# Kernel optimization log

Hardware: AMD Instinct MI355X
Metric: run time of the kernel (lower is better)

The kernel has to match this reference:

```python
import jax, jax.numpy as jnp
import numpy as np

B = 524288          # batch
C = 128             # num_classes
CONF_PEN = 0.5      # confusion_penalty coefficient
PROB_THRESH = 0.2   # wrong-prob threshold from original loop
WEIGHT_THRESH = 1.0 # weight threshold from original loop


def setup_inputs() -> dict:
    key = jax.random.key(0)
    k1, k2, k3 = jax.random.split(key, 3)
    # scale logits so softmax is peaky enough that the >0.2 branch fires
    outputs = 5.0 * jax.random.normal(k1, (B, C), dtype=jnp.float32)
    labels = jax.random.randint(k2, (B,), 0, C, dtype=jnp.int32)
    # uniform in [0, 2): roughly half the weights exceed the 1.0 threshold
    confusion_weights = jax.random.uniform(k3, (C, C), dtype=jnp.float32, minval=0.0, maxval=2.0)
    return {"outputs": outputs, "labels": labels, "confusion_weights": confusion_weights}


def reference(outputs, labels, confusion_weights):
    # base cross-entropy (mean over batch), numerically stable
    logp = jax.nn.log_softmax(outputs, axis=-1)                       # [B, C]
    base_loss = -jnp.take_along_axis(logp, labels[:, None].astype(jnp.int32), axis=1).mean()

    # confusion penalty (computed under no_grad in the original)
    probs = jnp.exp(logp)                                             # [B, C]
    w = confusion_weights[labels]                                     # [B, C] row per true label
    cls = jnp.arange(outputs.shape[1])
    mask = (cls[None, :] != labels[:, None]) & (w > WEIGHT_THRESH) & (probs > PROB_THRESH)
    pen_sum = jnp.sum(jnp.where(mask, w * probs, jnp.float32(0.0)))
    count = jnp.sum(mask)
    penalty = jnp.where(count > 0, pen_sum / jnp.maximum(count, 1).astype(pen_sum.dtype), jnp.float32(0.0))
    penalty = jax.lax.stop_gradient(penalty)  # mirrors torch.no_grad block

    return base_loss + CONF_PEN * penalty
```

## Files before the change

kernel.cpp:

```cpp
#include <hip/hip_runtime.h>

#define B_ROWS 524288
#define C_CLS  128
#define CONF_PEN 0.5f
#define PROB_THRESH 0.2f
#define WEIGHT_THRESH 1.0f

#define BLOCKS 2048
#define THREADS 256
#define WPB (THREADS / 64)
#define PAIRS 4
#define NWAVES (BLOCKS * WPB)
#define SWEEP (NWAVES * 2 * PAIRS)
#define ITERS (B_ROWS / SWEEP)

template <int CTRL>
__device__ __forceinline__ float dpp_add(float x) {
    int y = __builtin_amdgcn_update_dpp(0, __float_as_int(x), CTRL, 0xF, 0xF, true);
    return x + __int_as_float(y);
}
__device__ __forceinline__ float sum32(float s) {
    s = dpp_add<0xB1>(s);
    s = dpp_add<0x4E>(s);
    s = dpp_add<0x141>(s);
    s = dpp_add<0x140>(s);
    s += __shfl_xor(s, 16);
    return s;
}

__global__ __launch_bounds__(THREADS) void afl_prep(
    const float* __restrict__ cw, float* __restrict__ cwp) {
    const int i = blockIdx.x * THREADS + threadIdx.x;
    const int r = i >> 7, c = i & 127;
    const float w = cw[i];
    cwp[i] = (c != r && w > WEIGHT_THRESH) ? w : 0.0f;
}

__global__ __launch_bounds__(THREADS, 3) void afl_main(
    const float* __restrict__ outputs,
    const int* __restrict__ labels,
    const float* __restrict__ cwp,
    float* __restrict__ partial) {

    const int lane = threadIdx.x & 63;
    const int wave = threadIdx.x >> 6;
    const int half = lane >> 5;
    const int sub  = lane & 31;
    const int gwave = blockIdx.x * WPB + wave;
    const int row0  = gwave * (2 * PAIRS);

    float base_acc = 0.0f, pen_acc = 0.0f, cnt_acc = 0.0f;

    int    labc[PAIRS], labn[PAIRS];
    float4 vc[PAIRS];
    #pragma unroll
    for (int j = 0; j < PAIRS; ++j)
        labc[j] = labels[row0 + 2 * j + half];
    #pragma unroll
    for (int j = 0; j < PAIRS; ++j)
        labn[j] = labels[row0 + SWEEP + 2 * j + half];
    #pragma unroll
    for (int j = 0; j < PAIRS; ++j)
        vc[j] = ((const float4*)(outputs + (size_t)(row0 + 2 * j + half) * C_CLS))[sub];

    for (int it = 0; it < ITERS; ++it) {
        const int base = row0 + it * SWEEP;

        float4 w[PAIRS];
        #pragma unroll
        for (int j = 0; j < PAIRS; ++j)
            w[j] = ((const float4*)(cwp + (size_t)labc[j] * C_CLS))[sub];

        float4 vn[PAIRS];
        int    lab2[PAIRS];
        if (it + 1 < ITERS) {
            #pragma unroll
            for (int j = 0; j < PAIRS; ++j)
                vn[j] = ((const float4*)(outputs + (size_t)(base + SWEEP + 2 * j + half) * C_CLS))[sub];
        }
        if (it + 2 < ITERS) {
            #pragma unroll
            for (int j = 0; j < PAIRS; ++j)
                lab2[j] = labels[base + 2 * SWEEP + 2 * j + half];
        }

        #pragma unroll
        for (int j = 0; j < PAIRS; ++j) {
            const float e0 = __expf(vc[j].x);
            const float e1 = __expf(vc[j].y);
            const float e2 = __expf(vc[j].z);
            const float e3 = __expf(vc[j].w);
            float s = (e0 + e1) + (e2 + e3);
            s = sum32(s);

            const float thr   = PROB_THRESH * s;
            const float inv_s = __builtin_amdgcn_rcpf(s);
            const float logZ  = __logf(s);

            if ((labc[j] >> 2) == sub) {
                const float xl = (labc[j] & 2) ? ((labc[j] & 1) ? vc[j].w : vc[j].z)
                                               : ((labc[j] & 1) ? vc[j].y : vc[j].x);
                base_acc += logZ - xl;
            }

            float ps = 0.0f;
            ps = fmaf(w[j].x, (e0 > thr) ? e0 : 0.0f, ps);
            ps = fmaf(w[j].y, (e1 > thr) ? e1 : 0.0f, ps);
            ps = fmaf(w[j].z, (e2 > thr) ? e2 : 0.0f, ps);
            ps = fmaf(w[j].w, (e3 > thr) ? e3 : 0.0f, ps);
            pen_acc = fmaf(ps, inv_s, pen_acc);

            cnt_acc += ((w[j].x != 0.0f) && (e0 > thr)) ? 1.0f : 0.0f;
            cnt_acc += ((w[j].y != 0.0f) && (e1 > thr)) ? 1.0f : 0.0f;
            cnt_acc += ((w[j].z != 0.0f) && (e2 > thr)) ? 1.0f : 0.0f;
            cnt_acc += ((w[j].w != 0.0f) && (e3 > thr)) ? 1.0f : 0.0f;
        }

        if (it + 1 < ITERS) {
            #pragma unroll
            for (int j = 0; j < PAIRS; ++j) { vc[j] = vn[j]; labc[j] = labn[j]; }
            if (it + 2 < ITERS) {
                #pragma unroll
                for (int j = 0; j < PAIRS; ++j) labn[j] = lab2[j];
            }
        }
    }

    #pragma unroll
    for (int off = 32; off >= 1; off >>= 1) {
        base_acc += __shfl_xor(base_acc, off);
        pen_acc  += __shfl_xor(pen_acc, off);
        cnt_acc  += __shfl_xor(cnt_acc, off);
    }

    __shared__ float s_base[WPB], s_pen[WPB], s_cnt[WPB];
    if (lane == 0) { s_base[wave] = base_acc; s_pen[wave] = pen_acc; s_cnt[wave] = cnt_acc; }
    __syncthreads();
    if (threadIdx.x == 0) {
        float b = 0.0f, pn = 0.0f, c = 0.0f;
        #pragma unroll
        for (int i = 0; i < WPB; ++i) { b += s_base[i]; pn += s_pen[i]; c += s_cnt[i]; }
        partial[3 * blockIdx.x + 0] = b;
        partial[3 * blockIdx.x + 1] = pn;
        partial[3 * blockIdx.x + 2] = c;
    }
}

__global__ __launch_bounds__(256) void afl_finalize(
    const float* __restrict__ partial, float* __restrict__ out) {
    float b = 0.0f, pn = 0.0f, c = 0.0f;
    for (int i = threadIdx.x; i < BLOCKS; i += 256) {
        b  += partial[3 * i + 0];
        pn += partial[3 * i + 1];
        c  += partial[3 * i + 2];
    }
    #pragma unroll
    for (int off = 32; off >= 1; off >>= 1) {
        b  += __shfl_xor(b, off);
        pn += __shfl_xor(pn, off);
        c  += __shfl_xor(c, off);
    }
    __shared__ float sb[4], sp[4], sc[4];
    const int wave = threadIdx.x >> 6;
    if ((threadIdx.x & 63) == 0) { sb[wave] = b; sp[wave] = pn; sc[wave] = c; }
    __syncthreads();
    if (threadIdx.x == 0) {
        b  = sb[0] + sb[1] + sb[2] + sb[3];
        pn = sp[0] + sp[1] + sp[2] + sp[3];
        c  = sc[0] + sc[1] + sc[2] + sc[3];
        const float penalty = (c > 0.0f) ? (pn / c) : 0.0f;
        out[0] = b * (1.0f / (float)B_ROWS) + CONF_PEN * penalty;
    }
}

extern "C" void kernel_launch(void* const* d_in, const int* in_sizes, int n_in,
                              void* d_out, int out_size, void* d_ws, size_t ws_size,
                              hipStream_t stream) {
    const float* outputs = (const float*)d_in[0];
    const int*   labels  = (const int*)d_in[1];
    const float* cw      = (const float*)d_in[2];
    float* out     = (float*)d_out;
    float* partial = (float*)d_ws;
    float* cwp     = (float*)d_ws + 16384;

    afl_prep<<<(C_CLS * C_CLS) / THREADS, THREADS, 0, stream>>>(cw, cwp);
    afl_main<<<BLOCKS, THREADS, 0, stream>>>(outputs, labels, cwp, partial);
    afl_finalize<<<1, 256, 0, stream>>>(partial, out);
}
```

Baseline: 360.5 us.

## Drop prep kernel and software prefetch; load confusion weights only when prob passes threshold

Removes the separate prep kernel that pre-masked the confusion-weight matrix, and reads raw weights inside the main kernel only for elements whose probability exceeds the threshold. It also drops the manual double-buffered prefetch of logits and labels. Labels are now loaded with one load per wave and broadcast by shuffle, and the occupancy hint in launch bounds is removed. The aim is to cut one launch and the full per-row weight-row loads, at the cost of divergent scattered gathers and less latency hiding on the logits stream.

```diff
diff --git a/kernel.cpp b/kernel.cpp
--- a/kernel.cpp
+++ b/kernel.cpp
@@ -28,18 +28,10 @@
     return s;
 }
 
-__global__ __launch_bounds__(THREADS) void afl_prep(
-    const float* __restrict__ cw, float* __restrict__ cwp) {
-    const int i = blockIdx.x * THREADS + threadIdx.x;
-    const int r = i >> 7, c = i & 127;
-    const float w = cw[i];
-    cwp[i] = (c != r && w > WEIGHT_THRESH) ? w : 0.0f;
-}
-
-__global__ __launch_bounds__(THREADS, 3) void afl_main(
+__global__ __launch_bounds__(THREADS) void afl_main(
     const float* __restrict__ outputs,
     const int* __restrict__ labels,
-    const float* __restrict__ cwp,
+    const float* __restrict__ cw,
     float* __restrict__ partial) {
 
     const int lane = threadIdx.x & 63;
@@ -51,78 +43,56 @@
 
     float base_acc = 0.0f, pen_acc = 0.0f, cnt_acc = 0.0f;
 
-    int    labc[PAIRS], labn[PAIRS];
-    float4 vc[PAIRS];
-    #pragma unroll
-    for (int j = 0; j < PAIRS; ++j)
-        labc[j] = labels[row0 + 2 * j + half];
-    #pragma unroll
-    for (int j = 0; j < PAIRS; ++j)
-        labn[j] = labels[row0 + SWEEP + 2 * j + half];
-    #pragma unroll
-    for (int j = 0; j < PAIRS; ++j)
-        vc[j] = ((const float4*)(outputs + (size_t)(row0 + 2 * j + half) * C_CLS))[sub];
-
     for (int it = 0; it < ITERS; ++it) {
         const int base = row0 + it * SWEEP;
 
-        float4 w[PAIRS];
+        const int labv = labels[base + (lane & 7)];
+
+        float4 v[PAIRS];
         #pragma unroll
         for (int j = 0; j < PAIRS; ++j)
-            w[j] = ((const float4*)(cwp + (size_t)labc[j] * C_CLS))[sub];
-
-        float4 vn[PAIRS];
-        int    lab2[PAIRS];
-        if (it + 1 < ITERS) {
-            #pragma unroll
-            for (int j = 0; j < PAIRS; ++j)
-                vn[j] = ((const float4*)(outputs + (size_t)(base + SWEEP + 2 * j + half) * C_CLS))[sub];
-        }
-        if (it + 2 < ITERS) {
-            #pragma unroll
-            for (int j = 0; j < PAIRS; ++j)
-                lab2[j] = labels[base + 2 * SWEEP + 2 * j + half];
-        }
+            v[j] = ((const float4*)(outputs + (size_t)(base + 2 * j + half) * C_CLS))[sub];
 
         #pragma unroll
         for (int j = 0; j < PAIRS; ++j) {
-            const float e0 = __expf(vc[j].x);
-            const float e1 = __expf(vc[j].y);
-            const float e2 = __expf(vc[j].z);
-            const float e3 = __expf(vc[j].w);
+            const int lab = __shfl(labv, 2 * j + half);
+
+            const float e0 = __expf(v[j].x);
+            const float e1 = __expf(v[j].y);
+            const float e2 = __expf(v[j].z);
+            const float e3 = __expf(v[j].w);
             float s = (e0 + e1) + (e2 + e3);
             s = sum32(s);
 
             const float thr   = PROB_THRESH * s;
             const float inv_s = __builtin_amdgcn_rcpf(s);
-            const float logZ  = __logf(s);
 
-            if ((labc[j] >> 2) == sub) {
-                const float xl = (labc[j] & 2) ? ((labc[j] & 1) ? vc[j].w : vc[j].z)
-                                               : ((labc[j] & 1) ? vc[j].y : vc[j].x);
-                base_acc += logZ - xl;
+            if ((lab >> 2) == sub) {
+                const float xl = (lab & 2) ? ((lab & 1) ? v[j].w : v[j].z)
+                                           : ((lab & 1) ? v[j].y : v[j].x);
+                base_acc += __logf(s) - xl;
             }
 
+            const int c0 = 4 * sub;
+            const float* cwrow = cw + (size_t)lab * C_CLS;
             float ps = 0.0f;
-            ps = fmaf(w[j].x, (e0 > thr) ? e0 : 0.0f, ps);
-            ps = fmaf(w[j].y, (e1 > thr) ? e1 : 0.0f, ps);
-            ps = fmaf(w[j].z, (e2 > thr) ? e2 : 0.0f, ps);
-            ps = fmaf(w[j].w, (e3 > thr) ? e3 : 0.0f, ps);
+            if (e0 > thr && c0 + 0 != lab) {
+                const float wv = cwrow[c0 + 0];
+                if (wv > WEIGHT_THRESH) { ps = fmaf(wv, e0, ps); cnt_acc += 1.0f; }
+            }
+            if (e1 > thr && c0 + 1 != lab) {
+                const float wv = cwrow[c0 + 1];
+                if (wv > WEIGHT_THRESH) { ps = fmaf(wv, e1, ps); cnt_acc += 1.0f; }
+            }
+            if (e2 > thr && c0 + 2 != lab) {
+                const float wv = cwrow[c0 + 2];
+                if (wv > WEIGHT_THRESH) { ps = fmaf(wv, e2, ps); cnt_acc += 1.0f; }
+            }
+            if (e3 > thr && c0 + 3 != lab) {
+                const float wv = cwrow[c0 + 3];
+                if (wv > WEIGHT_THRESH) { ps = fmaf(wv, e3, ps); cnt_acc += 1.0f; }
+            }
             pen_acc = fmaf(ps, inv_s, pen_acc);
-
-            cnt_acc += ((w[j].x != 0.0f) && (e0 > thr)) ? 1.0f : 0.0f;
-            cnt_acc += ((w[j].y != 0.0f) && (e1 > thr)) ? 1.0f : 0.0f;
-            cnt_acc += ((w[j].z != 0.0f) && (e2 > thr)) ? 1.0f : 0.0f;
-            cnt_acc += ((w[j].w != 0.0f) && (e3 > thr)) ? 1.0f : 0.0f;
-        }
-
-        if (it + 1 < ITERS) {
-            #pragma unroll
-            for (int j = 0; j < PAIRS; ++j) { vc[j] = vn[j]; labc[j] = labn[j]; }
-            if (it + 2 < ITERS) {
-                #pragma unroll
-                for (int j = 0; j < PAIRS; ++j) labn[j] = lab2[j];
-            }
         }
     }
 
@@ -181,9 +151,7 @@
     const float* cw      = (const float*)d_in[2];
     float* out     = (float*)d_out;
     float* partial = (float*)d_ws;
-    float* cwp     = (float*)d_ws + 16384;
 
-    afl_prep<<<(C_CLS * C_CLS) / THREADS, THREADS, 0, stream>>>(cw, cwp);
-    afl_main<<<BLOCKS, THREADS, 0, stream>>>(outputs, labels, cwp, partial);
+    afl_main<<<BLOCKS, THREADS, 0, stream>>>(outputs, labels, cw, partial);
     afl_finalize<<<1, 256, 0, stream>>>(partial, out);
 }
```

After: 362.3 us. No clear change (+0.5%).
